# Optimization experiments

Measured on AMD Instinct MI355X. Metric: run time of the kernel, lower is better.

## Reference

```python
import jax, jax.numpy as jnp
import numpy as np

# HMS2 tiling configuration (matches init_kwargs)
TILE = 512          # tile_size in image pixels
CROP = 8            # emb_crop_size (in embedding pixels)
STRIDE = 4          # emb_stride_size: total downsampling of conv_module
OVERLAP = CROP * STRIDE * 2          # 64 image pixels
STEP = TILE - OVERLAP                # 448: stride between tile origins
IMG = 2304                           # image H = W; (IMG-TILE) % STEP == 0
NT = (IMG - TILE) // STEP + 1        # 5 tiles per axis
B = 1
E = TILE // STRIDE                   # 128: emb pixels per (uncropped) tile
DN = ('NHWC', 'HWIO', 'NHWC')


def conv_module(x, W1, b1, W2, b2):
    # Two stride-2 SAME convs with ReLU: total stride 4 (= emb_stride_size).
    x = jax.lax.conv_general_dilated(x, W1, (2, 2), 'SAME', dimension_numbers=DN) + b1
    x = jax.nn.relu(x)
    x = jax.lax.conv_general_dilated(x, W2, (2, 2), 'SAME', dimension_numbers=DN) + b2
    return jax.nn.relu(x)


def setup_inputs() -> dict:
    key = jax.random.key(0)
    k1, k2, k3 = jax.random.split(key, 3)
    image_batch = jax.random.randint(k1, (B, IMG, IMG, 3), 0, 256, dtype=jnp.int32)
    W1 = jax.random.normal(k2, (3, 3, 3, 64), dtype=jnp.float32) * 0.05
    b1 = jnp.zeros((64,), dtype=jnp.float32)
    W2 = jax.random.normal(k3, (3, 3, 64, 128), dtype=jnp.float32) * 0.05
    b2 = jnp.zeros((128,), dtype=jnp.float32)
    return {'image_batch': image_batch, 'W1': W1, 'b1': b1, 'W2': W2, 'b2': b2}


def reference(image_batch, W1, b1, W2, b2):
    # loader_module: slice tile from the big uint8 NHWC image, normalize to float.
    img = image_batch.astype(jnp.float32) / 255.0
    # Extract all overlapping tiles (static slices) -> [NT*NT, B, TILE, TILE, 3]
    tiles = jnp.stack([img[:, ty * STEP:ty * STEP + TILE, tx * STEP:tx * STEP + TILE, :]
                       for ty in range(NT) for tx in range(NT)])
    tiles = tiles.reshape(NT * NT * B, TILE, TILE, 3)
    emb = conv_module(tiles, W1, b1, W2, b2)          # [NT*NT*B, E, E, 128]
    emb = emb.reshape(NT, NT, B, E, E, -1)
    # Crop emb_crop_size on interior edges and stitch (as in _forward_tile).
    rows = []
    for ty in range(NT):
        top = 0 if ty == 0 else CROP
        bot = E if ty == NT - 1 else E - CROP
        cols = []
        for tx in range(NT):
            left = 0 if tx == 0 else CROP
            right = E if tx == NT - 1 else E - CROP
            cols.append(emb[ty, tx][:, top:bot, left:right, :])
        rows.append(jnp.concatenate(cols, axis=2))
    out = jnp.concatenate(rows, axis=1)               # [B, 576, 576, 128] NHWC
    return jnp.transpose(out, (0, 3, 1, 2))           # NCHW, matching torch emb
```

## Files before the change

### kernel.cpp

```cpp
#include <hip/hip_runtime.h>


#define IMG 2304
#define H1  1152
#define H2  576
#define C1  64
#define C2  128
#define TS  8
#define NTB (H2/TS)
#define C1T 17
#define IT  35
#define CPAD 40

typedef __bf16 bf16_t;
typedef __bf16 bf16x8 __attribute__((ext_vector_type(8)));
typedef __bf16 bf16x4 __attribute__((ext_vector_type(4)));
typedef _Float16 f16_t;
typedef _Float16 f16x8 __attribute__((ext_vector_type(8)));
typedef float  f32x16 __attribute__((ext_vector_type(16)));

#define W2T_BYTES (C2*576*2)

__global__ __launch_bounds__(256) void w2_transform(
    const float* __restrict__ W2, bf16_t* __restrict__ W2T)
{
    int idx  = blockIdx.x*256 + threadIdx.x;
    int ci   = idx & 31;
    int t    = idx >> 5;
    int kykx = t % 9;  t /= 9;
    int p    = t & 1;
    int n    = t >> 1;
    W2T[idx] = (bf16_t)W2[(size_t)(kykx*64 + p*32 + ci)*C2 + n];
}

__global__ __launch_bounds__(64) void w1_transform(
    const float* __restrict__ W1, const float* __restrict__ b1,
    f16_t* __restrict__ W1T)
{
    int oc = threadIdx.x;
    for (int k = 0; k < 32; ++k) {
        float v = 0.f;
        if (k < 27) v = W1[k*C1 + oc];
        else if (k == 27) v = b1[oc];
        W1T[oc*32 + k] = (f16_t)v;
    }
}

__global__ __launch_bounds__(256, 3) void hms2_fused(
    const int*    __restrict__ img,
    const float*  __restrict__ b2,
    const bf16_t* __restrict__ W2T,
    const f16_t*  __restrict__ W1T,
    float*        __restrict__ out)
{
    __shared__ __align__(16) char s_raw[48720];
    f16_t* s_i2c = (f16_t*)s_raw;
    float* s_img = (float*)(s_raw + 25600);
    char*  s_c1b = s_raw + 25600;
    float* s_ep  = (float*)s_raw;

    const int tid   = threadIdx.x;
    const int tileY = blockIdx.x / NTB;
    const int tileX = blockIdx.x % NTB;
    const int e0y = tileY*TS, e0x = tileX*TS;
    const int r0  = 2*e0y,    q0  = 2*e0x;
    const int iy0 = 4*e0y,    ix0 = 4*e0x;

    for (int i = tid; i < IT*IT*3; i += 256) {
        int ch = i % 3, pp = i / 3;
        int r = pp / IT, c = pp % IT;
        int gy = iy0 + r, gx = ix0 + c;
        float v = 0.f;
        if (gy < IMG && gx < IMG)
            v = (float)img[((size_t)gy*IMG + gx)*3 + ch] * (1.f/255.f);
        s_img[i] = v;
    }

    const int kcol = tid & 31;
    const int ky_ = kcol/9, krem = kcol - 9*ky_;
    const int kx_ = krem/3, ic_  = krem - 3*kx_;
    const int koff  = ky_*(IT*3) + kx_*3 + ic_;
    const bool kReal = (kcol < 27), kIs27 = (kcol == 27);

    __syncthreads();

    for (int idx = tid; idx < 320*32; idx += 256) {
        int s = idx >> 5;
        f16_t v = (f16_t)0.f;
        if (s < 289) {
            int r = s/17, q = s - 17*r;
            if (kReal)      v = (f16_t)s_img[(2*r*IT + 2*q)*3 + koff];
            else if (kIs27) v = (f16_t)1.f;
        }
        s_i2c[s*CPAD + kcol] = v;
    }

    const int lane = tid & 63;
    const int m    = lane & 31;
    const int kg   = lane >> 5;
    const int cg   = __builtin_amdgcn_readfirstlane(tid >> 6);

    const int h0  = m >> 3, w0 = m & 7;
    const int s00 = 34*h0 + 2*w0;
    const bf16_t* bBase = W2T + (size_t)(cg*32 + m)*576 + kg*8;

    f32x16 acc0, acc1;
    #pragma unroll
    for (int r = 0; r < 16; ++r) { acc0[r] = 0.f; acc1[r] = 0.f; }

    __syncthreads();

    #pragma unroll 1
    for (int p = 0; p < 2; ++p) {
        const f16_t* w1p = W1T + (size_t)(p*32 + m)*32 + kg*8;
        f16x8 wA = *(const f16x8*)(w1p);
        f16x8 wB = *(const f16x8*)(w1p + 16);

        for (int sf = cg; sf < 10; sf += 4) {
            const int n0 = sf*32;
            const f16_t* bp = s_i2c + (size_t)(n0 + m)*CPAD + kg*8;
            f16x8 i0 = *(const f16x8*)(bp);
            f16x8 i1 = *(const f16x8*)(bp + 16);
            f32x16 d;
            #pragma unroll
            for (int r = 0; r < 16; ++r) d[r] = 0.f;
            d = __builtin_amdgcn_mfma_f32_32x32x16_f16(wA, i0, d, 0, 0, 0);
            d = __builtin_amdgcn_mfma_f32_32x32x16_f16(wB, i1, d, 0, 0, 0);

            const int s = n0 + m;
            if (s < 289) {
                int rsp = s/17, qsp = s - 17*rsp;
                bool ok = (r0 + rsp < H1) && (q0 + qsp < H1);
                char* wp = s_c1b + s*80 + (((s>>3)&1)<<4) + kg*8;
                #pragma unroll
                for (int g = 0; g < 4; ++g) {
                    bf16x4 vv;
                    #pragma unroll
                    for (int jj = 0; jj < 4; ++jj) {
                        float x = fmaxf(d[4*g + jj], 0.f);
                        vv[jj] = ok ? (bf16_t)x : (bf16_t)0.f;
                    }
                    *(bf16x4*)(wp + g*16) = vv;
                }
            }
        }
        __syncthreads();

        const bf16_t* bP = bBase + p*288;
        #pragma unroll
        for (int kk = 0; kk < 9; ++kk) {
            const int dsh = (kk/3)*17 + (kk - 3*(kk/3));
            const int sA0 = s00 + dsh;
            const int sA1 = sA0 + 136;
            const int a0  = sA0*80 + (((sA0>>3)&1)<<4) + kg*16;
            const int a1  = sA1*80 + (((sA1>>3)&1)<<4) + kg*16;
            #pragma unroll
            for (int chh = 0; chh < 2; ++chh) {
                bf16x8 aF0 = *(const bf16x8*)(s_c1b + a0 + chh*32);
                bf16x8 aF1 = *(const bf16x8*)(s_c1b + a1 + chh*32);
                bf16x8 bF  = *(const bf16x8*)(bP + kk*32 + chh*16);
                acc0 = __builtin_amdgcn_mfma_f32_32x32x16_bf16(aF0, bF, acc0, 0, 0, 0);
                acc1 = __builtin_amdgcn_mfma_f32_32x32x16_bf16(aF1, bF, acc1, 0, 0, 0);
            }
        }
        __syncthreads();
    }

    {
        const int cOut = cg*32 + m;
        const float b2v = b2[cOut];
        #pragma unroll
        for (int r = 0; r < 16; ++r) {
            int row = (r&3) + 8*(r>>2) + 4*kg;
            s_ep[cOut*67 + row]      = fmaxf(acc0[r] + b2v, 0.f);
            s_ep[cOut*67 + 32 + row] = fmaxf(acc1[r] + b2v, 0.f);
        }
        __syncthreads();
        const int sp = tid & 63;
        const int gy = e0y + (sp >> 3), gx = e0x + (sp & 7);
        #pragma unroll
        for (int j = 0; j < 32; ++j) {
            int c = cg*32 + j;
            out[(size_t)c*(H2*H2) + (size_t)gy*H2 + gx] = s_ep[c*67 + sp];
        }
    }
}

extern "C" void kernel_launch(void* const* d_in, const int* in_sizes, int n_in,
                              void* d_out, int out_size, void* d_ws, size_t ws_size,
                              hipStream_t stream) {
    const int*   img = (const int*)  d_in[0];
    const float* W1  = (const float*)d_in[1];
    const float* b1  = (const float*)d_in[2];
    const float* W2  = (const float*)d_in[3];
    const float* b2  = (const float*)d_in[4];
    float*       out = (float*)d_out;
    bf16_t*      W2T = (bf16_t*)d_ws;
    f16_t*       W1T = (f16_t*)((char*)d_ws + W2T_BYTES);

    w2_transform<<<dim3(288), dim3(256), 0, stream>>>(W2, W2T);
    w1_transform<<<dim3(1),   dim3(64),  0, stream>>>(W1, b1, W1T);
    hms2_fused<<<dim3(NTB*NTB), dim3(256), 0, stream>>>(img, b2, W2T, W1T, out);
}
```

Baseline: 436.0 us.

## Swizzle LDS layouts, coalesce W2 fragment layout, and raise occupancy to 4 blocks

Replaces the padded im2col and conv1 LDS layouts with an XOR-style swizzled 128-byte-row layout, so padding is dropped and bank conflicts on the 16-byte fragment loads are avoided. Shared memory per block shrinks, and launch bounds now allow four resident blocks per CU instead of three. W2 is re-laid out so each lane's 8-element B fragment for a given k-slice sits contiguously across output channels, which makes the global loads coalesced. The risk is register pressure at the higher occupancy target and correctness of the swizzle indexing.

```diff
diff --git a/kernel.cpp b/kernel.cpp
--- a/kernel.cpp
+++ b/kernel.cpp
@@ -10,7 +10,6 @@
 #define NTB (H2/TS)
 #define C1T 17
 #define IT  35
-#define CPAD 40
 
 typedef __bf16 bf16_t;
 typedef __bf16 bf16x8 __attribute__((ext_vector_type(8)));
@@ -21,16 +20,21 @@
 
 #define W2T_BYTES (C2*576*2)
 
+#define SWZ(s, g) ( (((s)>>1)*128) + (((((g) + (((s)&1)<<2) + (((s)>>1)&7)) & 7)) << 4) )
+
 __global__ __launch_bounds__(256) void w2_transform(
     const float* __restrict__ W2, bf16_t* __restrict__ W2T)
 {
-    int idx  = blockIdx.x*256 + threadIdx.x;
-    int ci   = idx & 31;
-    int t    = idx >> 5;
-    int kykx = t % 9;  t /= 9;
-    int p    = t & 1;
-    int n    = t >> 1;
-    W2T[idx] = (bf16_t)W2[(size_t)(kykx*64 + p*32 + ci)*C2 + n];
+    int idx = blockIdx.x*256 + threadIdx.x;
+    int e   = idx & 7;
+    int t   = idx >> 3;
+    int n   = t & 127;  t >>= 7;
+    int oct = t & 3;    t >>= 2;
+    int kykx= t % 9;
+    int p   = t / 9;
+    int chh = oct >> 1, kg = oct & 1;
+    int ci64 = p*32 + chh*16 + kg*8 + e;
+    W2T[idx] = (bf16_t)W2[(size_t)(kykx*64 + ci64)*C2 + n];
 }
 
 __global__ __launch_bounds__(64) void w1_transform(
@@ -46,18 +50,18 @@
     }
 }
 
-__global__ __launch_bounds__(256, 3) void hms2_fused(
+__global__ __launch_bounds__(256, 4) void hms2_fused(
     const int*    __restrict__ img,
     const float*  __restrict__ b2,
     const bf16_t* __restrict__ W2T,
     const f16_t*  __restrict__ W1T,
     float*        __restrict__ out)
 {
-    __shared__ __align__(16) char s_raw[48720];
-    f16_t* s_i2c = (f16_t*)s_raw;
-    float* s_img = (float*)(s_raw + 25600);
-    char*  s_c1b = s_raw + 25600;
-    float* s_ep  = (float*)s_raw;
+    __shared__ __align__(16) char s_raw[39040];
+    char*  s_i2cb = s_raw;
+    float* s_img  = (float*)(s_raw + 20480);
+    char*  s_c1b  = s_raw + 20480;
+    float* s_ep   = (float*)s_raw;
 
     const int tid   = threadIdx.x;
     const int tileY = blockIdx.x / NTB;
@@ -92,7 +96,7 @@
             if (kReal)      v = (f16_t)s_img[(2*r*IT + 2*q)*3 + koff];
             else if (kIs27) v = (f16_t)1.f;
         }
-        s_i2c[s*CPAD + kcol] = v;
+        *(f16_t*)(s_i2cb + SWZ(s, kcol>>3) + (kcol&7)*2) = v;
     }
 
     const int lane = tid & 63;
@@ -102,7 +106,7 @@
 
     const int h0  = m >> 3, w0 = m & 7;
     const int s00 = 34*h0 + 2*w0;
-    const bf16_t* bBase = W2T + (size_t)(cg*32 + m)*576 + kg*8;
+    const bf16_t* bBase = W2T + (size_t)kg*1024 + (size_t)(cg*32 + m)*8;
 
     f32x16 acc0, acc1;
     #pragma unroll
@@ -117,21 +121,18 @@
         f16x8 wB = *(const f16x8*)(w1p + 16);
 
         for (int sf = cg; sf < 10; sf += 4) {
-            const int n0 = sf*32;
-            const f16_t* bp = s_i2c + (size_t)(n0 + m)*CPAD + kg*8;
-            f16x8 i0 = *(const f16x8*)(bp);
-            f16x8 i1 = *(const f16x8*)(bp + 16);
+            const int s = sf*32 + m;
+            f16x8 i0 = *(const f16x8*)(s_i2cb + SWZ(s, kg));
+            f16x8 i1 = *(const f16x8*)(s_i2cb + SWZ(s, kg+2));
             f32x16 d;
             #pragma unroll
             for (int r = 0; r < 16; ++r) d[r] = 0.f;
             d = __builtin_amdgcn_mfma_f32_32x32x16_f16(wA, i0, d, 0, 0, 0);
             d = __builtin_amdgcn_mfma_f32_32x32x16_f16(wB, i1, d, 0, 0, 0);
 
-            const int s = n0 + m;
             if (s < 289) {
                 int rsp = s/17, qsp = s - 17*rsp;
                 bool ok = (r0 + rsp < H1) && (q0 + qsp < H1);
-                char* wp = s_c1b + s*80 + (((s>>3)&1)<<4) + kg*8;
                 #pragma unroll
                 for (int g = 0; g < 4; ++g) {
                     bf16x4 vv;
@@ -140,25 +141,23 @@
                         float x = fmaxf(d[4*g + jj], 0.f);
                         vv[jj] = ok ? (bf16_t)x : (bf16_t)0.f;
                     }
-                    *(bf16x4*)(wp + g*16) = vv;
+                    *(bf16x4*)(s_c1b + SWZ(s, g) + kg*8) = vv;
                 }
             }
         }
         __syncthreads();
 
-        const bf16_t* bP = bBase + p*288;
+        const bf16_t* bP = bBase + (size_t)p*36*1024;
         #pragma unroll
         for (int kk = 0; kk < 9; ++kk) {
             const int dsh = (kk/3)*17 + (kk - 3*(kk/3));
             const int sA0 = s00 + dsh;
             const int sA1 = sA0 + 136;
-            const int a0  = sA0*80 + (((sA0>>3)&1)<<4) + kg*16;
-            const int a1  = sA1*80 + (((sA1>>3)&1)<<4) + kg*16;
             #pragma unroll
             for (int chh = 0; chh < 2; ++chh) {
-                bf16x8 aF0 = *(const bf16x8*)(s_c1b + a0 + chh*32);
-                bf16x8 aF1 = *(const bf16x8*)(s_c1b + a1 + chh*32);
-                bf16x8 bF  = *(const bf16x8*)(bP + kk*32 + chh*16);
+                bf16x8 aF0 = *(const bf16x8*)(s_c1b + SWZ(sA0, 2*chh + kg));
+                bf16x8 aF1 = *(const bf16x8*)(s_c1b + SWZ(sA1, 2*chh + kg));
+                bf16x8 bF  = *(const bf16x8*)(bP + (size_t)(kk*4 + chh*2)*1024);
                 acc0 = __builtin_amdgcn_mfma_f32_32x32x16_bf16(aF0, bF, acc0, 0, 0, 0);
                 acc1 = __builtin_amdgcn_mfma_f32_32x32x16_bf16(aF1, bF, acc1, 0, 0, 0);
             }
```

New measurement: 386.2 us. -11.4%, faster.
